# Kernel tuning notes

Hardware: AMD Instinct MI355X
Metric: run time of the kernel (lower is better)

The kernel has to match this reference:

```python
import jax, jax.numpy as jnp
import numpy as np

B, N, C, H = 256, 197, 768, 12
D = C // H  # 64
GRID = 14   # h = w = int(N**0.5); N-1 == 14*14


def setup_inputs() -> dict:
    key = jax.random.key(0)
    ks = jax.random.split(key, 5)
    s = 0.02
    return {
        "x": jax.random.normal(ks[0], (B, N, C), dtype=jnp.float32),
        "W_qkv": jax.random.normal(ks[1], (C, 3 * C), dtype=jnp.float32) * s,
        "b_qkv": jnp.zeros((3 * C,), dtype=jnp.float32),
        "W_proj": jax.random.normal(ks[2], (C, C), dtype=jnp.float32) * s,
        "b_proj": jnp.zeros((C,), dtype=jnp.float32),
        "dwc_w": jax.random.normal(ks[3], (C, 1, 3, 3), dtype=jnp.float32) * s,
        "dwc_b": jnp.zeros((C,), dtype=jnp.float32),
    }


def reference(x, W_qkv, b_qkv, W_proj, b_proj, dwc_w, dwc_b):
    Bx, Nx, Cx = x.shape
    Dh = Cx // H
    h = w = GRID
    # qkv projection -> (3, B, H, N, D)
    qkv = (x @ W_qkv + b_qkv).reshape(Bx, Nx, 3, H, Dh).transpose(2, 0, 3, 1, 4)
    q, k, v = qkv[0], qkv[1], qkv[2]
    scale = Dh ** -0.5
    # graph-candidate attention (softmax candidate): (B, H, N, N)
    attn = jax.nn.softmax(jnp.einsum('bhnd,bhmd->bhnm', q, k) * scale, axis=-1)
    out = jnp.einsum('bhnm,bhmd->bhnd', attn, v)
    out = out.transpose(0, 2, 1, 3).reshape(Bx, Nx, Cx)
    # depthwise conv on V (excluding cls token), residual add into rows 1:
    v_ = v[:, :, 1:, :].transpose(0, 2, 1, 3).reshape(Bx, h, w, Cx).transpose(0, 3, 1, 2)  # (B,C,h,w)
    conv = jax.lax.conv_general_dilated(
        v_, dwc_w, window_strides=(1, 1), padding='SAME',
        feature_group_count=Cx,
        dimension_numbers=('NCHW', 'OIHW', 'NCHW'),
    ) + dwc_b[None, :, None, None]
    out = out.at[:, 1:, :].add(conv.transpose(0, 2, 3, 1).reshape(Bx, Nx - 1, Cx))
    return out @ W_proj + b_proj
```

## Files before the change

kernel.cpp:

```cpp
#include <hip/hip_runtime.h>
#include <hip/hip_bf16.h>

typedef __attribute__((ext_vector_type(8))) short s16x8;
typedef __attribute__((ext_vector_type(4))) float f32x4;

#define MFMA(a, b, c) __builtin_amdgcn_mfma_f32_16x16x32_bf16((a), (b), (c), 0, 0, 0)

__device__ __forceinline__ short f2bf(float f) {
  unsigned u = __builtin_bit_cast(unsigned, f);
  u += 0x7FFFu + ((u >> 16) & 1u);
  return (short)(u >> 16);
}
__device__ __forceinline__ float bf2f(short s) {
  unsigned u = ((unsigned)(unsigned short)s) << 16;
  return __builtin_bit_cast(float, u);
}
__device__ __forceinline__ void async16(const void* g, void* l) {
  __builtin_amdgcn_global_load_lds((const __attribute__((address_space(1))) void*)g,
                                   (__attribute__((address_space(3))) void*)l, 16, 0, 0);
}


__global__ __launch_bounds__(256) void f32_to_bf16_k(const float* __restrict__ in,
                                                     short* __restrict__ out, int n4) {
  int i = blockIdx.x * 256 + threadIdx.x;
  if (i >= n4) return;
  float4 v = ((const float4*)in)[i];
  short4 o;
  o.x = f2bf(v.x); o.y = f2bf(v.y); o.z = f2bf(v.z); o.w = f2bf(v.w);
  ((short4*)out)[i] = o;
}

__global__ __launch_bounds__(256) void transpose_bf16_k(const float* __restrict__ in,
                                                        short* __restrict__ out, int K, int N) {
  int idx = blockIdx.x * 256 + threadIdx.x;
  if (idx >= K * N) return;
  int n = idx / K;
  int k = idx - n * K;
  out[idx] = f2bf(in[k * N + n]);
}


__device__ __forceinline__ void gemm_core(const short* __restrict__ A, const short* __restrict__ Bt,
                                          short* Asm, short* Bsm, int m0, int n0,
                                          f32x4 (&acc)[4][4]) {
  const int tid = threadIdx.x;
  const int lane = tid & 63;
  const int w = tid >> 6;
  const int wm = w >> 1, wn = w & 1;
  const int l15 = lane & 15, qd = lane >> 4;

  for (int kt = 0; kt < 12; ++kt) {
    __syncthreads();
#pragma unroll
    for (int i = 0; i < 4; ++i) {
      int s = i * 256 + tid;
      int row = s >> 3, cst = s & 7;
      int cg = cst ^ (row & 7);
      async16(A + (m0 + row) * 768 + kt * 64 + cg * 8, Asm + s * 8);
      async16(Bt + (n0 + row) * 768 + kt * 64 + cg * 8, Bsm + s * 8);
    }
    __builtin_amdgcn_s_waitcnt(0x0f70);
    __syncthreads();
#pragma unroll
    for (int ks = 0; ks < 2; ++ks) {
      s16x8 af[4], bfr[4];
#pragma unroll
      for (int mt = 0; mt < 4; ++mt) {
        int row = wm * 64 + mt * 16 + l15;
        int kc = ks * 4 + qd;
        af[mt] = *(const s16x8*)(Asm + row * 64 + ((kc ^ (row & 7)) << 3));
      }
#pragma unroll
      for (int nt = 0; nt < 4; ++nt) {
        int row = wn * 64 + nt * 16 + l15;
        int kc = ks * 4 + qd;
        bfr[nt] = *(const s16x8*)(Bsm + row * 64 + ((kc ^ (row & 7)) << 3));
      }
#pragma unroll
      for (int mt = 0; mt < 4; ++mt)
#pragma unroll
        for (int nt = 0; nt < 4; ++nt)
          acc[mt][nt] = MFMA(af[mt], bfr[nt], acc[mt][nt]);
    }
  }
}

__global__ __launch_bounds__(256) void gemm_qkv(const short* __restrict__ A, const short* __restrict__ Bt,
                                                const float* __restrict__ bias,
                                                short* __restrict__ qo, short* __restrict__ ko,
                                                short* __restrict__ vo) {
  __shared__ short Asm[128 * 64];
  __shared__ short Bsm[128 * 64];
  const int m0 = blockIdx.x * 128;
  const int n0 = blockIdx.y * 128;
  const f32x4 z4 = {0.f, 0.f, 0.f, 0.f};
  f32x4 acc[4][4];
#pragma unroll
  for (int i = 0; i < 4; ++i)
#pragma unroll
    for (int j = 0; j < 4; ++j) acc[i][j] = z4;
  gemm_core(A, Bt, Asm, Bsm, m0, n0, acc);

  const int tid = threadIdx.x, lane = tid & 63, w = tid >> 6;
  const int wm = w >> 1, wn = w & 1, l15 = lane & 15, qd = lane >> 4;

  float bv[4];
  short* dstp[4];
  int coff[4];
#pragma unroll
  for (int nt = 0; nt < 4; ++nt) {
    int n = n0 + wn * 64 + nt * 16 + l15;
    bv[nt] = bias[n];
    int s = n / 768;
    int rem = n - s * 768;
    int hh = rem >> 6, d = rem & 63;
    dstp[nt] = (s == 0) ? qo : ((s == 1) ? ko : vo);
    coff[nt] = hh * 197 * 64 + d;
  }
#pragma unroll
  for (int mt = 0; mt < 4; ++mt) {
#pragma unroll
    for (int r = 0; r < 4; ++r) {
      int m = m0 + wm * 64 + mt * 16 + qd * 4 + r;
      int bb = m / 197;
      int tok = m - bb * 197;
      size_t base = (size_t)bb * (12 * 197 * 64) + (size_t)tok * 64;
#pragma unroll
      for (int nt = 0; nt < 4; ++nt)
        dstp[nt][base + coff[nt]] = f2bf(acc[mt][nt][r] + bv[nt]);
    }
  }
}

__global__ __launch_bounds__(256) void gemm_proj(const short* __restrict__ A, const short* __restrict__ Bt,
                                                 const float* __restrict__ bias,
                                                 float* __restrict__ out) {
  __shared__ short Asm[128 * 64];
  __shared__ short Bsm[128 * 64];
  const int m0 = blockIdx.x * 128;
  const int n0 = blockIdx.y * 128;
  const f32x4 z4 = {0.f, 0.f, 0.f, 0.f};
  f32x4 acc[4][4];
#pragma unroll
  for (int i = 0; i < 4; ++i)
#pragma unroll
    for (int j = 0; j < 4; ++j) acc[i][j] = z4;
  gemm_core(A, Bt, Asm, Bsm, m0, n0, acc);

  const int tid = threadIdx.x, lane = tid & 63, w = tid >> 6;
  const int wm = w >> 1, wn = w & 1, l15 = lane & 15, qd = lane >> 4;
#pragma unroll
  for (int mt = 0; mt < 4; ++mt) {
#pragma unroll
    for (int r = 0; r < 4; ++r) {
      int m = m0 + wm * 64 + mt * 16 + qd * 4 + r;
      float* orow = out + (size_t)m * 768;
#pragma unroll
      for (int nt = 0; nt < 4; ++nt) {
        int n = n0 + wn * 64 + nt * 16 + l15;
        orow[n] = acc[mt][nt][r] + bias[n];
      }
    }
  }
}

__global__ __launch_bounds__(256) void attn_fused(const short* __restrict__ qa, const short* __restrict__ ka,
                                                  const short* __restrict__ va,
                                                  const float* __restrict__ dwcw,
                                                  const float* __restrict__ dwcb,
                                                  short* __restrict__ aout) {
  __shared__ short Klds[197 * 64];
  __shared__ short Vt[64 * 256];
  __shared__ short Plds[4][16 * 40];
  __shared__ float Wc[576];

  const int tid = threadIdx.x;
  const int lane = tid & 63;
  const int w = tid >> 6;
  const int l15 = lane & 15, qd = lane >> 4;
  const int bh = blockIdx.x;
  const int b = bh / 12;
  const int h = bh - b * 12;
  const short* kb = ka + (size_t)bh * (197 * 64);
  const short* vb = va + (size_t)bh * (197 * 64);
  const short* qb = qa + (size_t)bh * (197 * 64);

  for (int c = tid; c < 197 * 8; c += 256) {
    int row = c >> 3, cc = c & 7;
    s16x8 v8 = *(const s16x8*)(kb + row * 64 + cc * 8);
    *(s16x8*)(Klds + row * 64 + ((cc ^ (row & 7)) << 3)) = v8;
  }
  for (int c = tid; c < 197 * 8; c += 256) {
    int key = c >> 3, cc = c & 7;
    s16x8 v8 = *(const s16x8*)(vb + key * 64 + cc * 8);
    int kc = key >> 3, km = key & 7;
#pragma unroll
    for (int j = 0; j < 8; ++j) {
      int d = cc * 8 + j;
      Vt[d * 256 + ((kc ^ (d & 7)) << 3) + km] = v8[j];
    }
  }
  for (int i = tid; i < 64 * 27; i += 256) {
    int d = i / 27;
    int key = 197 + (i - d * 27);
    Vt[d * 256 + (((key >> 3) ^ (d & 7)) << 3) + (key & 7)] = 0;
  }
  for (int i = tid; i < 576; i += 256) Wc[i] = dwcw[h * 576 + i];
  __syncthreads();

  float cbv[4];
#pragma unroll
  for (int nt = 0; nt < 4; ++nt) cbv[nt] = dwcb[h * 64 + nt * 16 + l15];

  for (int qt = w; qt < 13; qt += 4) {
    const int m0 = qt * 16;
    int mrow = m0 + l15; if (mrow > 196) mrow = 196;
    s16x8 qf0 = *(const s16x8*)(qb + mrow * 64 + qd * 8);
    s16x8 qf1 = *(const s16x8*)(qb + mrow * 64 + 32 + qd * 8);

    f32x4 S[13];
#pragma unroll
    for (int kt = 0; kt < 13; ++kt) {
      int krow = kt * 16 + l15; if (krow > 196) krow = 196;
      s16x8 kf0 = *(const s16x8*)(Klds + krow * 64 + ((qd ^ (krow & 7)) << 3));
      s16x8 kf1 = *(const s16x8*)(Klds + krow * 64 + (((4 + qd) ^ (krow & 7)) << 3));
      f32x4 sa = {0.f, 0.f, 0.f, 0.f};
      sa = MFMA(qf0, kf0, sa);
      sa = MFMA(qf1, kf1, sa);
      S[kt] = sa;
    }
    const bool maskme = (l15 > 4);
#pragma unroll
    for (int kt = 0; kt < 13; ++kt) {
#pragma unroll
      for (int r = 0; r < 4; ++r) {
        float sv = S[kt][r] * 0.125f;
        if (kt == 12 && maskme) sv = -1e30f;
        S[kt][r] = sv;
      }
    }
    float li[4];
#pragma unroll
    for (int r = 0; r < 4; ++r) {
      float m = S[0][r];
#pragma unroll
      for (int kt = 1; kt < 13; ++kt) m = fmaxf(m, S[kt][r]);
#pragma unroll
      for (int off = 1; off < 16; off <<= 1) m = fmaxf(m, __shfl_xor(m, off));
      float l = 0.f;
#pragma unroll
      for (int kt = 0; kt < 13; ++kt) {
        float p = __builtin_amdgcn_exp2f((S[kt][r] - m) * 1.44269504f);
        S[kt][r] = p;
        l += p;
      }
#pragma unroll
      for (int off = 1; off < 16; off <<= 1) l += __shfl_xor(l, off);
      li[r] = l;
    }

    const f32x4 z4 = {0.f, 0.f, 0.f, 0.f};
    f32x4 O[4] = {z4, z4, z4, z4};
    short* Pw = &Plds[w][0];
#pragma unroll
    for (int kt2 = 0; kt2 < 7; ++kt2) {
#pragma unroll
      for (int sub = 0; sub < 2; ++sub) {
        const int ktile = kt2 * 2 + sub;
#pragma unroll
        for (int r = 0; r < 4; ++r) {
          short pv = 0;
          if (ktile < 13) pv = f2bf(S[ktile][r]);
          Pw[(qd * 4 + r) * 40 + sub * 16 + l15] = pv;
        }
      }
      __builtin_amdgcn_s_waitcnt(0xc07f);
      s16x8 pf = *(const s16x8*)(Pw + l15 * 40 + qd * 8);
#pragma unroll
      for (int nt = 0; nt < 4; ++nt) {
        int d = nt * 16 + l15;
        s16x8 vf = *(const s16x8*)(Vt + d * 256 + (((kt2 * 4 + qd) ^ (d & 7)) << 3));
        O[nt] = MFMA(pf, vf, O[nt]);
      }
    }

#pragma unroll
    for (int r = 0; r < 4; ++r) {
      int tok = m0 + qd * 4 + r;
      if (tok > 196) continue;
      float linv = __builtin_amdgcn_rcpf(li[r]);
      int py = 0, px = 0;
      const bool dconv = (tok >= 1);
      if (dconv) { int p = tok - 1; py = p / 14; px = p - py * 14; }
      size_t ob = ((size_t)b * 197 + tok) * 768 + h * 64;
#pragma unroll
      for (int nt = 0; nt < 4; ++nt) {
        int d = nt * 16 + l15;
        float val = O[nt][r] * linv;
        if (dconv) {
          float cv = cbv[nt];
#pragma unroll
          for (int dy = -1; dy <= 1; ++dy) {
            int yy = py + dy;
#pragma unroll
            for (int dx = -1; dx <= 1; ++dx) {
              int xx = px + dx;
              if (yy >= 0 && yy < 14 && xx >= 0 && xx < 14) {
                int key = 1 + yy * 14 + xx;
                float vv = bf2f(Vt[d * 256 + (((key >> 3) ^ (d & 7)) << 3) + (key & 7)]);
                cv += Wc[d * 9 + (dy + 1) * 3 + (dx + 1)] * vv;
              }
            }
          }
          val += cv;
        }
        aout[ob + d] = f2bf(val);
      }
    }
  }
}


extern "C" void kernel_launch(void* const* d_in, const int* in_sizes, int n_in,
                              void* d_out, int out_size, void* d_ws, size_t ws_size,
                              hipStream_t stream) {
  const float* x     = (const float*)d_in[0];
  const float* Wqkv  = (const float*)d_in[1];
  const float* bqkv  = (const float*)d_in[2];
  const float* Wproj = (const float*)d_in[3];
  const float* bproj = (const float*)d_in[4];
  const float* dwcw  = (const float*)d_in[5];
  const float* dwcb  = (const float*)d_in[6];
  float* out = (float*)d_out;

  const size_t XE = (size_t)50432 * 768;
  short* ws     = (short*)d_ws;
  short* xbf    = ws;
  short* wqkvT  = xbf + XE;
  short* wprojT = wqkvT + (size_t)2304 * 768;
  short* qarr   = wprojT + (size_t)768 * 768;
  short* karr   = qarr + XE;
  short* varr   = karr + XE;
  short* aoutb  = xbf;

  f32_to_bf16_k<<<(int)((XE / 4 + 255) / 256), 256, 0, stream>>>(x, xbf, (int)(XE / 4));
  transpose_bf16_k<<<(2304 * 768 + 255) / 256, 256, 0, stream>>>(Wqkv, wqkvT, 768, 2304);
  transpose_bf16_k<<<(768 * 768 + 255) / 256, 256, 0, stream>>>(Wproj, wprojT, 768, 768);
  gemm_qkv<<<dim3(394, 18), 256, 0, stream>>>(xbf, wqkvT, bqkv, qarr, karr, varr);
  attn_fused<<<3072, 256, 0, stream>>>(qarr, karr, varr, dwcw, dwcb, aoutb);
  gemm_proj<<<dim3(394, 6), 256, 0, stream>>>(aoutb, wprojT, bproj, out);
}
```

Measured before the change: 970.4 us.

## Restructure attention kernel: transposed S, in-register P, separate conv pass, swapped GEMM grid

Swaps the GEMM grid so blockIdx.x walks N tiles, which should improve reuse of A tiles in L2. The attention kernel now uses 512 threads, loads K asynchronously into LDS, and builds V^T with packed 4-element stores. It computes S transposed so each lane holds one query column, which lets softmax reduce with two shuffles and feed P straight from registers into 16x16x16 MFMAs instead of staging through LDS. The depthwise conv moves to a separate phase that reads V from global memory and does a read-modify-write on the output, adding extra global traffic and an extra bf16 rounding.

```diff
diff --git a/kernel.cpp b/kernel.cpp
--- a/kernel.cpp
+++ b/kernel.cpp
@@ -2,9 +2,21 @@
 #include <hip/hip_bf16.h>
 
 typedef __attribute__((ext_vector_type(8))) short s16x8;
+typedef __attribute__((ext_vector_type(4))) short s16x4;
 typedef __attribute__((ext_vector_type(4))) float f32x4;
 
 #define MFMA(a, b, c) __builtin_amdgcn_mfma_f32_16x16x32_bf16((a), (b), (c), 0, 0, 0)
+
+#if __has_builtin(__builtin_amdgcn_mfma_f32_16x16x16bf16_1k)
+#define MFMA16(a, b, c) __builtin_amdgcn_mfma_f32_16x16x16bf16_1k((a), (b), (c), 0, 0, 0)
+#else
+__device__ __forceinline__ f32x4 mfma16_asm(s16x4 a, s16x4 b, f32x4 c) {
+  asm volatile("v_mfma_f32_16x16x16_bf16 %0, %1, %2, %0\n\ts_nop 7\n\ts_nop 7"
+               : "+v"(c) : "v"(a), "v"(b));
+  return c;
+}
+#define MFMA16(a, b, c) mfma16_asm((a), (b), (c))
+#endif
 
 __device__ __forceinline__ short f2bf(float f) {
   unsigned u = __builtin_bit_cast(unsigned, f);
@@ -92,8 +104,8 @@
                                                 short* __restrict__ vo) {
   __shared__ short Asm[128 * 64];
   __shared__ short Bsm[128 * 64];
-  const int m0 = blockIdx.x * 128;
-  const int n0 = blockIdx.y * 128;
+  const int m0 = blockIdx.y * 128;
+  const int n0 = blockIdx.x * 128;
   const f32x4 z4 = {0.f, 0.f, 0.f, 0.f};
   f32x4 acc[4][4];
 #pragma unroll
@@ -138,8 +150,8 @@
                                                  float* __restrict__ out) {
   __shared__ short Asm[128 * 64];
   __shared__ short Bsm[128 * 64];
-  const int m0 = blockIdx.x * 128;
-  const int n0 = blockIdx.y * 128;
+  const int m0 = blockIdx.y * 128;
+  const int n0 = blockIdx.x * 128;
   const f32x4 z4 = {0.f, 0.f, 0.f, 0.f};
   f32x4 acc[4][4];
 #pragma unroll
@@ -165,15 +177,13 @@
   }
 }
 
-__global__ __launch_bounds__(256) void attn_fused(const short* __restrict__ qa, const short* __restrict__ ka,
-                                                  const short* __restrict__ va,
-                                                  const float* __restrict__ dwcw,
-                                                  const float* __restrict__ dwcb,
-                                                  short* __restrict__ aout) {
+__global__ __launch_bounds__(512, 4) void attn_fused(const short* __restrict__ qa, const short* __restrict__ ka,
+                                                     const short* __restrict__ va,
+                                                     const float* __restrict__ dwcw,
+                                                     const float* __restrict__ dwcb,
+                                                     short* __restrict__ aout) {
   __shared__ short Klds[197 * 64];
   __shared__ short Vt[64 * 256];
-  __shared__ short Plds[4][16 * 40];
-  __shared__ float Wc[576];
 
   const int tid = threadIdx.x;
   const int lane = tid & 63;
@@ -186,34 +196,29 @@
   const short* vb = va + (size_t)bh * (197 * 64);
   const short* qb = qa + (size_t)bh * (197 * 64);
 
-  for (int c = tid; c < 197 * 8; c += 256) {
-    int row = c >> 3, cc = c & 7;
-    s16x8 v8 = *(const s16x8*)(kb + row * 64 + cc * 8);
-    *(s16x8*)(Klds + row * 64 + ((cc ^ (row & 7)) << 3)) = v8;
-  }
-  for (int c = tid; c < 197 * 8; c += 256) {
-    int key = c >> 3, cc = c & 7;
-    s16x8 v8 = *(const s16x8*)(vb + key * 64 + cc * 8);
-    int kc = key >> 3, km = key & 7;
-#pragma unroll
-    for (int j = 0; j < 8; ++j) {
-      int d = cc * 8 + j;
-      Vt[d * 256 + ((kc ^ (d & 7)) << 3) + km] = v8[j];
-    }
-  }
-  for (int i = tid; i < 64 * 27; i += 256) {
-    int d = i / 27;
-    int key = 197 + (i - d * 27);
-    Vt[d * 256 + (((key >> 3) ^ (d & 7)) << 3) + (key & 7)] = 0;
-  }
-  for (int i = tid; i < 576; i += 256) Wc[i] = dwcw[h * 576 + i];
+  for (int s = tid; s < 197 * 8; s += 512) {
+    int row = s >> 3, cst = s & 7;
+    int cg = cst ^ (row & 7);
+    async16(kb + row * 64 + cg * 8, Klds + s * 8);
+  }
+  for (int t = tid; t < 64 * 52; t += 512) {
+    int d = t & 63, kc4 = t >> 6;
+    s16x4 pack;
+#pragma unroll
+    for (int j = 0; j < 4; ++j) {
+      int key = kc4 * 4 + j;
+      pack[j] = (key <= 196) ? vb[key * 64 + d] : (short)0;
+    }
+    int kc8 = kc4 >> 1, sub = (kc4 & 1) * 4;
+    *(s16x4*)(Vt + d * 256 + ((kc8 ^ (d & 7)) << 3) + sub) = pack;
+  }
+  __builtin_amdgcn_s_waitcnt(0x0f70);
   __syncthreads();
 
-  float cbv[4];
-#pragma unroll
-  for (int nt = 0; nt < 4; ++nt) cbv[nt] = dwcb[h * 64 + nt * 16 + l15];
-
-  for (int qt = w; qt < 13; qt += 4) {
+  const float scale_log2e = 0.125f * 1.44269504f;
+  const f32x4 z4 = {0.f, 0.f, 0.f, 0.f};
+
+  for (int qt = w; qt < 13; qt += 8) {
     const int m0 = qt * 16;
     int mrow = m0 + l15; if (mrow > 196) mrow = 196;
     s16x8 qf0 = *(const s16x8*)(qb + mrow * 64 + qd * 8);
@@ -225,63 +230,50 @@
       int krow = kt * 16 + l15; if (krow > 196) krow = 196;
       s16x8 kf0 = *(const s16x8*)(Klds + krow * 64 + ((qd ^ (krow & 7)) << 3));
       s16x8 kf1 = *(const s16x8*)(Klds + krow * 64 + (((4 + qd) ^ (krow & 7)) << 3));
-      f32x4 sa = {0.f, 0.f, 0.f, 0.f};
-      sa = MFMA(qf0, kf0, sa);
-      sa = MFMA(qf1, kf1, sa);
+      f32x4 sa = z4;
+      sa = MFMA(kf0, qf0, sa);
+      sa = MFMA(kf1, qf1, sa);
       S[kt] = sa;
     }
-    const bool maskme = (l15 > 4);
+#pragma unroll
+    for (int r = 0; r < 4; ++r)
+      if (qd * 4 + r > 4) S[12][r] = -3.0e38f;
+
+    float mx = -3.0e38f;
+#pragma unroll
+    for (int kt = 0; kt < 13; ++kt)
+#pragma unroll
+      for (int r = 0; r < 4; ++r) mx = fmaxf(mx, S[kt][r]);
+    mx = fmaxf(mx, __shfl_xor(mx, 16));
+    mx = fmaxf(mx, __shfl_xor(mx, 32));
+
+    float l = 0.f;
 #pragma unroll
     for (int kt = 0; kt < 13; ++kt) {
 #pragma unroll
       for (int r = 0; r < 4; ++r) {
-        float sv = S[kt][r] * 0.125f;
-        if (kt == 12 && maskme) sv = -1e30f;
-        S[kt][r] = sv;
-      }
-    }
-    float li[4];
-#pragma unroll
-    for (int r = 0; r < 4; ++r) {
-      float m = S[0][r];
-#pragma unroll
-      for (int kt = 1; kt < 13; ++kt) m = fmaxf(m, S[kt][r]);
-#pragma unroll
-      for (int off = 1; off < 16; off <<= 1) m = fmaxf(m, __shfl_xor(m, off));
-      float l = 0.f;
-#pragma unroll
-      for (int kt = 0; kt < 13; ++kt) {
-        float p = __builtin_amdgcn_exp2f((S[kt][r] - m) * 1.44269504f);
+        float p = __builtin_amdgcn_exp2f((S[kt][r] - mx) * scale_log2e);
         S[kt][r] = p;
         l += p;
       }
-#pragma unroll
-      for (int off = 1; off < 16; off <<= 1) l += __shfl_xor(l, off);
-      li[r] = l;
-    }
-
-    const f32x4 z4 = {0.f, 0.f, 0.f, 0.f};
+    }
+    l += __shfl_xor(l, 16);
+    l += __shfl_xor(l, 32);
+    float linv = __builtin_amdgcn_rcpf(l);
+
     f32x4 O[4] = {z4, z4, z4, z4};
-    short* Pw = &Plds[w][0];
-#pragma unroll
-    for (int kt2 = 0; kt2 < 7; ++kt2) {
-#pragma unroll
-      for (int sub = 0; sub < 2; ++sub) {
-        const int ktile = kt2 * 2 + sub;
-#pragma unroll
-        for (int r = 0; r < 4; ++r) {
-          short pv = 0;
-          if (ktile < 13) pv = f2bf(S[ktile][r]);
-          Pw[(qd * 4 + r) * 40 + sub * 16 + l15] = pv;
-        }
-      }
-      __builtin_amdgcn_s_waitcnt(0xc07f);
-      s16x8 pf = *(const s16x8*)(Pw + l15 * 40 + qd * 8);
+#pragma unroll
+    for (int kt = 0; kt < 13; ++kt) {
+      s16x4 a4;
+#pragma unroll
+      for (int r = 0; r < 4; ++r) a4[r] = f2bf(S[kt][r] * linv);
+      int kc8b = kt * 2 + (qd >> 1);
+      int sub = (qd & 1) * 4;
 #pragma unroll
       for (int nt = 0; nt < 4; ++nt) {
         int d = nt * 16 + l15;
-        s16x8 vf = *(const s16x8*)(Vt + d * 256 + (((kt2 * 4 + qd) ^ (d & 7)) << 3));
-        O[nt] = MFMA(pf, vf, O[nt]);
+        s16x4 vf = *(const s16x4*)(Vt + d * 256 + ((kc8b ^ (d & 7)) << 3) + sub);
+        O[nt] = MFMA16(a4, vf, O[nt]);
       }
     }
 
@@ -289,33 +281,54 @@
     for (int r = 0; r < 4; ++r) {
       int tok = m0 + qd * 4 + r;
       if (tok > 196) continue;
-      float linv = __builtin_amdgcn_rcpf(li[r]);
-      int py = 0, px = 0;
-      const bool dconv = (tok >= 1);
-      if (dconv) { int p = tok - 1; py = p / 14; px = p - py * 14; }
       size_t ob = ((size_t)b * 197 + tok) * 768 + h * 64;
 #pragma unroll
-      for (int nt = 0; nt < 4; ++nt) {
-        int d = nt * 16 + l15;
-        float val = O[nt][r] * linv;
-        if (dconv) {
-          float cv = cbv[nt];
-#pragma unroll
-          for (int dy = -1; dy <= 1; ++dy) {
-            int yy = py + dy;
-#pragma unroll
-            for (int dx = -1; dx <= 1; ++dx) {
-              int xx = px + dx;
-              if (yy >= 0 && yy < 14 && xx >= 0 && xx < 14) {
-                int key = 1 + yy * 14 + xx;
-                float vv = bf2f(Vt[d * 256 + (((key >> 3) ^ (d & 7)) << 3) + (key & 7)]);
-                cv += Wc[d * 9 + (dy + 1) * 3 + (dx + 1)] * vv;
-              }
-            }
+      for (int nt = 0; nt < 4; ++nt)
+        aout[ob + nt * 16 + l15] = f2bf(O[nt][r]);
+    }
+  }
+
+  __syncthreads();
+
+  {
+    const int d = tid & 63;
+    const int seg = tid >> 6;
+    float wreg[9];
+#pragma unroll
+    for (int tp = 0; tp < 9; ++tp) wreg[tp] = dwcw[(h * 64 + d) * 9 + tp];
+    const float breg = dwcb[h * 64 + d];
+
+    for (int c = seg; c < 28; c += 8) {
+      int y = c >> 1;
+      int xb = (c & 1) * 8;
+      int xn = (c & 1) ? 6 : 8;
+      float vv[3][10];
+#pragma unroll
+      for (int dy = 0; dy < 3; ++dy) {
+        int yy = y - 1 + dy;
+#pragma unroll
+        for (int k = 0; k < 10; ++k) {
+          int xx = xb - 1 + k;
+          float val = 0.f;
+          if (yy >= 0 && yy < 14 && xx >= 0 && xx < 14) {
+            int key = 1 + yy * 14 + xx;
+            val = bf2f(vb[key * 64 + d]);
           }
-          val += cv;
+          vv[dy][k] = val;
         }
-        aout[ob + d] = f2bf(val);
+      }
+#pragma unroll
+      for (int x = 0; x < 8; ++x) {
+        if (x >= xn) break;
+        float acc = breg;
+#pragma unroll
+        for (int dy = 0; dy < 3; ++dy)
+#pragma unroll
+          for (int dx = 0; dx < 3; ++dx)
+            acc += wreg[dy * 3 + dx] * vv[dy][x + dx];
+        int tok = 1 + y * 14 + xb + x;
+        size_t oa = ((size_t)b * 197 + tok) * 768 + h * 64 + d;
+        aout[oa] = f2bf(bf2f(aout[oa]) + acc);
       }
     }
   }
@@ -347,7 +360,7 @@
   f32_to_bf16_k<<<(int)((XE / 4 + 255) / 256), 256, 0, stream>>>(x, xbf, (int)(XE / 4));
   transpose_bf16_k<<<(2304 * 768 + 255) / 256, 256, 0, stream>>>(Wqkv, wqkvT, 768, 2304);
   transpose_bf16_k<<<(768 * 768 + 255) / 256, 256, 0, stream>>>(Wproj, wprojT, 768, 768);
-  gemm_qkv<<<dim3(394, 18), 256, 0, stream>>>(xbf, wqkvT, bqkv, qarr, karr, varr);
-  attn_fused<<<3072, 256, 0, stream>>>(qarr, karr, varr, dwcw, dwcb, aoutb);
-  gemm_proj<<<dim3(394, 6), 256, 0, stream>>>(aoutb, wprojT, bproj, out);
-}
+  gemm_qkv<<<dim3(18, 394), 256, 0, stream>>>(xbf, wqkvT, bqkv, qarr, karr, varr);
+  attn_fused<<<3072, 512, 0, stream>>>(qarr, karr, varr, dwcw, dwcb, aoutb);
+  gemm_proj<<<dim3(6, 394), 256, 0, stream>>>(aoutb, wprojT, bproj, out);
+}
```

New measurement: 1.386 ms. +42.8%, slower.
